# Kernel optimization log

Measured on AMD Instinct MI355X. Metric: run time of the kernel, lower is better.

Reference implementation:

```python
import jax, jax.numpy as jnp
import numpy as np
from jax import lax

DN = ('NCHW', 'OIHW', 'NCHW')

def _conv(x, w, pad):
    return lax.conv_general_dilated(x, w, (1, 1), [(pad, pad), (pad, pad)], dimension_numbers=DN)

def _bn(x, g, b, eps=1e-5):
    # BatchNorm2d in training mode: batch statistics over (N,H,W), biased variance
    m = jnp.mean(x, axis=(0, 2, 3), keepdims=True)
    v = jnp.var(x, axis=(0, 2, 3), keepdims=True)
    return (x - m) * lax.rsqrt(v + eps) * g.reshape(1, -1, 1, 1) + b.reshape(1, -1, 1, 1)

def setup_inputs() -> dict:
    key = jax.random.key(0)
    ks = jax.random.split(key, 24)
    B, H, W = 128, 64, 64
    l_i, lh = 2, (150, 120, 100)
    l_q, cf = 10, H * W
    r = lambda k, s, sc: jax.random.normal(k, s, dtype=jnp.float32) * sc
    return {
        'X': r(ks[0], (B, l_i, H, W), 1.0),
        'obs': r(ks[1], (B, 24), 1.0),
        'h1_w': r(ks[2], (lh[0], l_i, 3, 3), 0.1), 'h1_b': r(ks[3], (lh[0],), 0.05),
        'g1': jnp.ones((lh[0],), jnp.float32), 'b1': jnp.zeros((lh[0],), jnp.float32),
        'h2_w': r(ks[4], (lh[1], lh[0], 3, 3), 0.03), 'h2_b': r(ks[5], (lh[1],), 0.05),
        'g2': jnp.ones((lh[1],), jnp.float32), 'b2': jnp.zeros((lh[1],), jnp.float32),
        'h3_w': r(ks[6], (lh[2], lh[1], 3, 3), 0.03), 'h3_b': r(ks[7], (lh[2],), 0.05),
        'g3': jnp.ones((lh[2],), jnp.float32), 'b3': jnp.zeros((lh[2],), jnp.float32),
        'r_w': r(ks[8], (1, lh[2], 1, 1), 0.1),
        'q_w': r(ks[9], (l_q, 1, 5, 5), 0.1),
        'w': r(ks[10], (l_q, 1, 5, 5), 0.05),  # Parameter (zeros init in torch; randn here for nontrivial math)
        'fc1_w': r(ks[11], (100, 24), 0.1), 'fc1_b': r(ks[12], (100,), 0.05),
        'fc2_w': r(ks[13], (10, 100), 0.1), 'fc2_b': r(ks[14], (10,), 0.05),
        'cv_w': r(ks[15], (1, cf), 0.02), 'cv_b': r(ks[16], (1,), 0.05),
        'K': 36,
    }

def reference(X, obs, h1_w, h1_b, g1, b1, h2_w, h2_b, g2, b2, h3_w, h3_b, g3, b3,
              r_w, q_w, w, fc1_w, fc1_b, fc2_w, fc2_b, cv_w, cv_b, K):
    relu = jax.nn.relu
    h = relu(_bn(_conv(X, h1_w, 1) + h1_b.reshape(1, -1, 1, 1), g1, b1))
    h = relu(_bn(_conv(h, h2_w, 1) + h2_b.reshape(1, -1, 1, 1), g2, b2))
    h = relu(_bn(_conv(h, h3_w, 1) + h3_b.reshape(1, -1, 1, 1), g3, b3))
    r = _conv(h, r_w, 0)                      # [B,1,H,W] reward map
    qr = _conv(r, q_w, 2)                     # conv of r part is constant across VI iterations
    v = jnp.max(qr, axis=1, keepdims=True)    # [B,1,H,W]
    # conv2d(cat([r,v],1), cat([q_w,w],1)) == conv(r,q_w) + conv(v,w)
    def step(v, _):
        q = qr + _conv(v, w, 2)
        return jnp.max(q, axis=1, keepdims=True), None
    # original: K-1 loop iterations + 1 extra conv/max = K total steps after the init
    v, _ = lax.scan(step, v, None, length=K)
    critic = v.reshape(v.shape[0], -1) @ cv_w.T + cv_b
    action_pred = relu(relu(obs @ fc1_w.T + fc1_b) @ fc2_w.T + fc2_b)
    return (critic, action_pred)
```

## Files before the change

### kernel.cpp

```cpp
#include <hip/hip_runtime.h>


#define NHW 524288.0f

typedef __attribute__((ext_vector_type(8))) short v8s;
typedef __attribute__((ext_vector_type(4))) float v4f;

static __device__ __forceinline__ float bf2f(unsigned short u) {
  return __uint_as_float(((unsigned int)u) << 16);
}
static __device__ __forceinline__ unsigned short f2bf(float f) {
  unsigned int x = __float_as_uint(f);
  return (unsigned short)((x + 0x7fffu + ((x >> 16) & 1u)) >> 16);
}
static __device__ __forceinline__ float wave_sum(float s) {
  #pragma unroll
  for (int off = 32; off > 0; off >>= 1) s += __shfl_down(s, off, 64);
  return s;
}

template <int CO, int CI, int CIP>
__global__ __launch_bounds__(256) void repack_w(
    const float* __restrict__ w, unsigned short* __restrict__ Wp)
{
  int i = blockIdx.x * 256 + threadIdx.x;
  const int total = 9 * 128 * CIP;
  if (i >= total) return;
  int pos = i / (128 * CIP);
  int rem = i - pos * (128 * CIP);
  int co  = rem / CIP;
  int ci  = rem - co * CIP;
  float v = (co < CO && ci < CI) ? w[(co * CI + ci) * 9 + pos] : 0.f;
  Wp[i] = f2bf(v);
}

__global__ __launch_bounds__(256) void conv1_stats(
    const float* __restrict__ X, const float* __restrict__ w1,
    const float* __restrict__ b1, float* __restrict__ S, float* __restrict__ Q)
{
  const int tile = blockIdx.x;
  const int b    = tile >> 3;
  const int y0t  = (tile & 7) * 8;
  const int co0  = blockIdx.y * 15;
  const int tid  = threadIdx.x;
  const int x    = tid & 63;
  const int ly0  = (tid >> 6) * 2;

  __shared__ float lin[2][10][66];
  __shared__ float ss[15], qq[15];
  if (tid < 15) { ss[tid] = 0.f; qq[tid] = 0.f; }
  for (int idx = tid; idx < 2 * 10 * 66; idx += 256) {
    int cc = idx / 660, rem = idx - cc * 660;
    int rr = rem / 66,  c   = rem - rr * 66;
    int yy = y0t + rr - 1, xx = c - 1;
    lin[cc][rr][c] = (yy >= 0 && yy < 64 && xx >= 0 && xx < 64)
                         ? X[((size_t)(b * 2 + cc) << 12) + (yy << 6) + xx] : 0.f;
  }
  __syncthreads();

  float iv[2][4][3];
  #pragma unroll
  for (int cc = 0; cc < 2; cc++)
    #pragma unroll
    for (int r = 0; r < 4; r++)
      #pragma unroll
      for (int c = 0; c < 3; c++) iv[cc][r][c] = lin[cc][ly0 + r][x + c];

  #pragma unroll
  for (int co = 0; co < 15; co++) {
    const float* w9 = w1 + (size_t)(co0 + co) * 18;
    float a0 = 0.f, a1 = 0.f;
    #pragma unroll
    for (int cc = 0; cc < 2; cc++)
      #pragma unroll
      for (int ky = 0; ky < 3; ky++)
        #pragma unroll
        for (int kx = 0; kx < 3; kx++) {
          float wv = w9[cc * 9 + ky * 3 + kx];
          a0 = fmaf(iv[cc][ky][kx],     wv, a0);
          a1 = fmaf(iv[cc][ky + 1][kx], wv, a1);
        }
    float bz = b1[co0 + co];
    float t0 = a0 + bz, t1 = a1 + bz;
    float s  = wave_sum(t0 + t1);
    float q  = wave_sum(t0 * t0 + t1 * t1);
    if ((tid & 63) == 0) { atomicAdd(&ss[co], s); atomicAdd(&qq[co], q); }
  }
  __syncthreads();
  if (tid < 15) {
    atomicAdd(&S[co0 + tid], ss[tid]);
    atomicAdd(&Q[co0 + tid], qq[tid]);
  }
}

template <int C>
__global__ void bn_finalize(const float* __restrict__ S, const float* __restrict__ Q,
                            const float* __restrict__ g, const float* __restrict__ be,
                            float* __restrict__ A, float* __restrict__ Bs)
{
  int c = threadIdx.x;
  if (c < C) {
    const float invN = 1.f / NHW;
    float m   = S[c] * invN;
    float var = fmaxf(Q[c] * invN - m * m, 0.f);
    float sc  = g[c] * rsqrtf(var + 1e-5f);
    A[c]  = sc;
    Bs[c] = be[c] - m * sc;
  }
}

__global__ __launch_bounds__(256, 2) void conv2_mfma(
    const float* __restrict__ X,  const float* __restrict__ w1,
    const float* __restrict__ b1f, const float* __restrict__ A1,
    const float* __restrict__ B1, const unsigned short* __restrict__ W2p,
    const float* __restrict__ b2, unsigned short* __restrict__ t2)
{
  const int bx   = blockIdx.x;
  const int b    = bx >> 4;
  const int t16  = bx & 15;
  const int y0   = (t16 >> 2) * 16;
  const int x0   = (t16 & 3) * 16;
  const int cg   = blockIdx.y;
  const int tid  = threadIdx.x;
  const int lane = tid & 63;
  const int wid  = __builtin_amdgcn_readfirstlane(tid >> 6);
  const int ln   = lane & 15;
  const int quad = (lane >> 4) * 8;

  __shared__ __align__(16) float Xs[2][20][20];
  __shared__ float w1s[2700];
  __shared__ float A1s[150], B1s[150], b1s[150], b2s[64];
  __shared__ __align__(16) unsigned short Atile[324 * 34];
  __shared__ __align__(16) unsigned short Btile[9 * 64 * 34];

  for (int i = tid; i < 2700; i += 256) w1s[i] = w1[i];
  for (int i = tid; i < 150; i += 256) { A1s[i] = A1[i]; B1s[i] = B1[i]; b1s[i] = b1f[i]; }
  if (tid < 64) { int co = cg * 64 + tid; b2s[tid] = (co < 120) ? b2[co] : 0.f; }
  for (int i = tid; i < 800; i += 256) {
    int c2 = i / 400, rem = i - c2 * 400;
    int rr = rem / 20, cc = rem - rr * 20;
    int gy = y0 - 2 + rr, gx = x0 - 2 + cc;
    Xs[c2][rr][cc] = (gy >= 0 && gy < 64 && gx >= 0 && gx < 64)
                         ? X[((size_t)(b * 2 + c2) << 12) + (gy << 6) + gx] : 0.f;
  }

  v4f acc[4][4];
  #pragma unroll
  for (int i = 0; i < 4; i++)
    #pragma unroll
    for (int j = 0; j < 4; j++) acc[i][j] = (v4f){0.f, 0.f, 0.f, 0.f};

  for (int chunk = 0; chunk < 5; chunk++) {
    __syncthreads();
    {
      const int ci_loc = tid & 31;
      const int ci = chunk * 32 + ci_loc;
      const bool live = (ci < 150);
      float wv[18], sc = 0.f, sh = 0.f, bz = 0.f;
      if (live) {
        #pragma unroll
        for (int k = 0; k < 18; k++) wv[k] = w1s[ci * 18 + k];
        sc = A1s[ci]; sh = B1s[ci]; bz = b1s[ci];
      }
      for (int pass = 0; pass < 41; pass++) {
        int p = pass * 8 + (tid >> 5);
        if (p < 324) {
          float v = 0.f;
          if (live) {
            int pr = p / 18, pc = p - pr * 18;
            int hy = y0 - 1 + pr, hx = x0 - 1 + pc;
            if (hy >= 0 && hy < 64 && hx >= 0 && hx < 64) {
              float a = bz;
              #pragma unroll
              for (int c2 = 0; c2 < 2; c2++)
                #pragma unroll
                for (int ky = 0; ky < 3; ky++)
                  #pragma unroll
                  for (int kx = 0; kx < 3; kx++)
                    a = fmaf(Xs[c2][pr + ky][pc + kx], wv[c2 * 9 + ky * 3 + kx], a);
              v = fmaxf(fmaf(a, sc, sh), 0.f);
            }
          }
          Atile[p * 34 + ci_loc] = f2bf(v);
        }
      }
    }
    for (int i = tid; i < 2304; i += 256) {
      int pos = i >> 8, rem = i & 255, co = rem >> 2, q = rem & 3;
      uint4 v = *(const uint4*)(W2p + (size_t)(pos * 128 + cg * 64 + co) * 160
                                + chunk * 32 + q * 8);
      *(uint4*)(&Btile[(pos * 64 + co) * 34 + q * 8]) = v;
    }
    __syncthreads();

    v8s afr[6][3];
    #pragma unroll
    for (int t = 0; t < 6; t++)
      #pragma unroll
      for (int kx = 0; kx < 3; kx++)
        afr[t][kx] = *(const v8s*)(&Atile[((wid * 4 + t) * 18 + ln + kx) * 34 + quad]);

    #pragma unroll
    for (int pos = 0; pos < 9; pos++) {
      const int ky = pos / 3, kx = pos - ky * 3;
      v8s bf[4];
      #pragma unroll
      for (int nj = 0; nj < 4; nj++)
        bf[nj] = *(const v8s*)(&Btile[(pos * 64 + nj * 16 + ln) * 34 + quad]);
      #pragma unroll
      for (int mi = 0; mi < 4; mi++) {
        #pragma unroll
        for (int nj = 0; nj < 4; nj++)
          acc[mi][nj] = __builtin_amdgcn_mfma_f32_16x16x32_bf16(
              afr[mi + ky][kx], bf[nj], acc[mi][nj], 0, 0, 0);
      }
    }
  }
  __syncthreads();

  unsigned short* outs = Btile;
  #pragma unroll
  for (int mi = 0; mi < 4; mi++)
    #pragma unroll
    for (int nj = 0; nj < 4; nj++) {
      int n = nj * 16 + ln;
      float bz = b2s[n];
      #pragma unroll
      for (int r2 = 0; r2 < 4; r2++) {
        int m = wid * 64 + mi * 16 + (lane >> 4) * 4 + r2;
        outs[m * 68 + n] = f2bf(acc[mi][nj][r2] + bz);
      }
    }
  __syncthreads();

  const int ng = cg ? 7 : 8;
  for (int i = tid; i < 256 * ng; i += 256) {
    int p = i / ng, g = i - p * ng;
    int gy = y0 + (p >> 4), gx = x0 + (p & 15);
    size_t gpx = ((size_t)b << 12) + (gy << 6) + gx;
    *(uint4*)(t2 + gpx * 120 + cg * 64 + g * 8) = *(const uint4*)(&outs[p * 68 + g * 8]);
  }
}

__global__ __launch_bounds__(256, 2) void conv3_mfma(
    const unsigned short* __restrict__ t2, const float* __restrict__ A2,
    const float* __restrict__ B2, const unsigned short* __restrict__ W3p,
    const float* __restrict__ b3, unsigned short* __restrict__ t3)
{
  const int bx   = blockIdx.x;
  const int b    = bx >> 4;
  const int t16  = bx & 15;
  const int y0   = (t16 >> 2) * 16;
  const int x0   = (t16 & 3) * 16;
  const int cg   = blockIdx.y;
  const int tid  = threadIdx.x;
  const int lane = tid & 63;
  const int wid  = __builtin_amdgcn_readfirstlane(tid >> 6);
  const int ln   = lane & 15;
  const int quad = (lane >> 4) * 8;

  __shared__ float A2s[120], B2s[120], b3s[64];
  __shared__ __align__(16) unsigned short Atile[324 * 34];
  __shared__ __align__(16) unsigned short Btile[9 * 64 * 34];

  for (int i = tid; i < 120; i += 256) { A2s[i] = A2[i]; B2s[i] = B2[i]; }
  if (tid < 64) { int co = cg * 64 + tid; b3s[tid] = (co < 100) ? b3[co] : 0.f; }

  v4f acc[4][4];
  #pragma unroll
  for (int i = 0; i < 4; i++)
    #pragma unroll
    for (int j = 0; j < 4; j++) acc[i][j] = (v4f){0.f, 0.f, 0.f, 0.f};

  for (int chunk = 0; chunk < 4; chunk++) {
    __syncthreads();
    {
      const int ci0 = chunk * 32;
      const int ngr = (chunk == 3) ? 3 : 4;
      for (int i = tid; i < 1296; i += 256) {
        int p = i >> 2, g = i & 3;
        int pr = p / 18, pc = p - pr * 18;
        int hy = y0 - 1 + pr, hx = x0 - 1 + pc;
        union { uint4 v; unsigned short u[8]; } ov;
        ov.v = (uint4){0, 0, 0, 0};
        if (g < ngr && hy >= 0 && hy < 64 && hx >= 0 && hx < 64) {
          size_t gpx = ((size_t)b << 12) + (hy << 6) + hx;
          union { uint4 v; unsigned short u[8]; } in;
          in.v = *(const uint4*)(t2 + gpx * 120 + ci0 + g * 8);
          #pragma unroll
          for (int j = 0; j < 8; j++) {
            int ci = ci0 + g * 8 + j;
            ov.u[j] = f2bf(fmaxf(fmaf(bf2f(in.u[j]), A2s[ci], B2s[ci]), 0.f));
          }
        }
        *(uint4*)(&Atile[p * 34 + g * 8]) = ov.v;
      }
    }
    for (int i = tid; i < 2304; i += 256) {
      int pos = i >> 8, rem = i & 255, co = rem >> 2, q = rem & 3;
      uint4 v = *(const uint4*)(W3p + (size_t)(pos * 128 + cg * 64 + co) * 128
                                + chunk * 32 + q * 8);
      *(uint4*)(&Btile[(pos * 64 + co) * 34 + q * 8]) = v;
    }
    __syncthreads();

    v8s afr[6][3];
    #pragma unroll
    for (int t = 0; t < 6; t++)
      #pragma unroll
      for (int kx = 0; kx < 3; kx++)
        afr[t][kx] = *(const v8s*)(&Atile[((wid * 4 + t) * 18 + ln + kx) * 34 + quad]);

    #pragma unroll
    for (int pos = 0; pos < 9; pos++) {
      const int ky = pos / 3, kx = pos - ky * 3;
      v8s bf[4];
      #pragma unroll
      for (int nj = 0; nj < 4; nj++)
        bf[nj] = *(const v8s*)(&Btile[(pos * 64 + nj * 16 + ln) * 34 + quad]);
      #pragma unroll
      for (int mi = 0; mi < 4; mi++) {
        #pragma unroll
        for (int nj = 0; nj < 4; nj++)
          acc[mi][nj] = __builtin_amdgcn_mfma_f32_16x16x32_bf16(
              afr[mi + ky][kx], bf[nj], acc[mi][nj], 0, 0, 0);
      }
    }
  }
  __syncthreads();

  unsigned short* outs = Btile;
  #pragma unroll
  for (int mi = 0; mi < 4; mi++)
    #pragma unroll
    for (int nj = 0; nj < 4; nj++) {
      int n = nj * 16 + ln;
      float bz = b3s[n];
      #pragma unroll
      for (int r2 = 0; r2 < 4; r2++) {
        int m = wid * 64 + mi * 16 + (lane >> 4) * 4 + r2;
        outs[m * 68 + n] = f2bf(acc[mi][nj][r2] + bz);
      }
    }
  __syncthreads();

  const int ng = cg ? 5 : 8;
  for (int i = tid; i < 256 * ng; i += 256) {
    int p = i / ng, g = i - p * ng;
    int gy = y0 + (p >> 4), gx = x0 + (p & 15);
    size_t gpx = ((size_t)b << 12) + (gy << 6) + gx;
    *(uint4*)(t3 + gpx * 104 + cg * 64 + g * 8) = *(const uint4*)(&outs[p * 68 + g * 8]);
  }
}

template <int ST, int NG, int C>
__global__ __launch_bounds__(256) void nhwc_stats(
    const unsigned short* __restrict__ t, float* __restrict__ S, float* __restrict__ Q)
{
  const int tid = threadIdx.x;
  const int g   = tid & 15;
  const int pl  = tid >> 4;
  const bool valid = (g < NG);
  const int px0 = blockIdx.x * 512;

  __shared__ float ss[128], qq[128];
  for (int i = tid; i < 128; i += 256) { ss[i] = 0.f; qq[i] = 0.f; }
  __syncthreads();

  float s8[8], q8[8];
  #pragma unroll
  for (int j = 0; j < 8; j++) { s8[j] = 0.f; q8[j] = 0.f; }

  if (valid) {
    for (int it = 0; it < 32; it++) {
      size_t px = px0 + it * 16 + pl;
      union { uint4 v; unsigned short u[8]; } in;
      in.v = *(const uint4*)(t + px * ST + g * 8);
      #pragma unroll
      for (int j = 0; j < 8; j++) {
        float v = bf2f(in.u[j]);
        s8[j] += v;
        q8[j] += v * v;
      }
    }
    #pragma unroll
    for (int j = 0; j < 8; j++) {
      atomicAdd(&ss[g * 8 + j], s8[j]);
      atomicAdd(&qq[g * 8 + j], q8[j]);
    }
  }
  __syncthreads();
  if (tid < C) {
    atomicAdd(&S[tid], ss[tid]);
    atomicAdd(&Q[tid], qq[tid]);
  }
}

__global__ __launch_bounds__(256) void bn3_reduce_r(
    const unsigned short* __restrict__ t3, const float* __restrict__ A3,
    const float* __restrict__ B3, const float* __restrict__ rw,
    float* __restrict__ r)
{
  __shared__ float A3s[104], B3s[104], rws[104];
  const int tid = threadIdx.x;
  for (int i = tid; i < 104; i += 256) {
    bool v = (i < 100);
    A3s[i] = v ? A3[i] : 0.f;
    B3s[i] = v ? B3[i] : 0.f;
    rws[i] = v ? rw[i] : 0.f;
  }
  __syncthreads();

  size_t px = (size_t)blockIdx.x * 256 + tid;
  const unsigned short* p = t3 + px * 104;
  float a = 0.f;
  #pragma unroll
  for (int gq = 0; gq < 13; gq++) {
    union { uint4 v; unsigned short u[8]; } in;
    in.v = *(const uint4*)(p + gq * 8);
    #pragma unroll
    for (int j = 0; j < 8; j++) {
      int ci = gq * 8 + j;
      a = fmaf(fmaxf(fmaf(bf2f(in.u[j]), A3s[ci], B3s[ci]), 0.f), rws[ci], a);
    }
  }
  r[px] = a;
}

__global__ __launch_bounds__(256) void qr_init(
    const float* __restrict__ r, const float* __restrict__ qw,
    float* __restrict__ qr, float* __restrict__ v0)
{
  const int tile = blockIdx.x;
  const int b    = tile >> 4;
  const int y0t  = (tile & 15) * 4;
  const int tid  = threadIdx.x;
  const int x    = tid & 63;
  const int ly   = tid >> 6;

  __shared__ float lv[8][68];
  for (int idx = tid; idx < 8 * 68; idx += 256) {
    int rr = idx / 68, c = idx - rr * 68;
    int yy = y0t + rr - 2, xx = c - 2;
    lv[rr][c] = (yy >= 0 && yy < 64 && xx >= 0 && xx < 64)
                    ? r[((size_t)b << 12) + (yy << 6) + xx] : 0.f;
  }
  __syncthreads();

  float iv[5][5];
  #pragma unroll
  for (int ky = 0; ky < 5; ky++)
    #pragma unroll
    for (int kx = 0; kx < 5; kx++) iv[ky][kx] = lv[ly + ky][x + kx];

  const int y = y0t + ly;
  float vmax = -1e30f;
  #pragma unroll
  for (int a = 0; a < 10; a++) {
    float q = 0.f;
    #pragma unroll
    for (int ky = 0; ky < 5; ky++)
      #pragma unroll
      for (int kx = 0; kx < 5; kx++)
        q = fmaf(iv[ky][kx], qw[a * 25 + ky * 5 + kx], q);
    qr[((size_t)(b * 10 + a) << 12) + (y << 6) + x] = q;
    vmax = fmaxf(vmax, q);
  }
  v0[((size_t)b << 12) + (y << 6) + x] = vmax;
}

__global__ __launch_bounds__(256) void vi_step(
    const float* __restrict__ vin, const float* __restrict__ qr,
    const float* __restrict__ ww, float* __restrict__ vout)
{
  const int tile = blockIdx.x;
  const int b    = tile >> 4;
  const int y0t  = (tile & 15) * 4;
  const int tid  = threadIdx.x;
  const int x    = tid & 63;
  const int ly   = tid >> 6;

  __shared__ float lv[8][68];
  for (int idx = tid; idx < 8 * 68; idx += 256) {
    int rr = idx / 68, c = idx - rr * 68;
    int yy = y0t + rr - 2, xx = c - 2;
    lv[rr][c] = (yy >= 0 && yy < 64 && xx >= 0 && xx < 64)
                    ? vin[((size_t)b << 12) + (yy << 6) + xx] : 0.f;
  }
  __syncthreads();

  float iv[5][5];
  #pragma unroll
  for (int ky = 0; ky < 5; ky++)
    #pragma unroll
    for (int kx = 0; kx < 5; kx++) iv[ky][kx] = lv[ly + ky][x + kx];

  const int y = y0t + ly;
  float vmax = -1e30f;
  #pragma unroll
  for (int a = 0; a < 10; a++) {
    float q = qr[((size_t)(b * 10 + a) << 12) + (y << 6) + x];
    #pragma unroll
    for (int ky = 0; ky < 5; ky++)
      #pragma unroll
      for (int kx = 0; kx < 5; kx++)
        q = fmaf(iv[ky][kx], ww[a * 25 + ky * 5 + kx], q);
    vmax = fmaxf(vmax, q);
  }
  vout[((size_t)b << 12) + (y << 6) + x] = vmax;
}

__global__ __launch_bounds__(256) void critic_k(
    const float* __restrict__ v, const float* __restrict__ cvw,
    const float* __restrict__ cvb, float* __restrict__ out)
{
  const int b = blockIdx.x;
  const int tid = threadIdx.x;
  const float4* pv = (const float4*)(v + ((size_t)b << 12));
  const float4* pw = (const float4*)cvw;
  float s = 0.f;
  #pragma unroll
  for (int i = 0; i < 4; i++) {
    float4 a = pv[tid + 256 * i];
    float4 w = pw[tid + 256 * i];
    s += a.x * w.x + a.y * w.y + a.z * w.z + a.w * w.w;
  }
  s = wave_sum(s);
  __shared__ float ls[4];
  const int w = tid >> 6;
  if ((tid & 63) == 0) ls[w] = s;
  __syncthreads();
  if (tid == 0) out[b] = ls[0] + ls[1] + ls[2] + ls[3] + cvb[0];
}

__global__ __launch_bounds__(128) void action_k(
    const float* __restrict__ obs, const float* __restrict__ fc1w,
    const float* __restrict__ fc1b, const float* __restrict__ fc2w,
    const float* __restrict__ fc2b, float* __restrict__ out)
{
  const int b = blockIdx.x;
  const int j = threadIdx.x;
  __shared__ float ob[24];
  __shared__ float h[100];
  if (j < 24) ob[j] = obs[b * 24 + j];
  __syncthreads();
  if (j < 100) {
    float s = fc1b[j];
    #pragma unroll
    for (int k = 0; k < 24; k++) s = fmaf(ob[k], fc1w[j * 24 + k], s);
    h[j] = fmaxf(s, 0.f);
  }
  __syncthreads();
  if (j < 10) {
    float s = fc2b[j];
    for (int k = 0; k < 100; k++) s = fmaf(h[k], fc2w[j * 100 + k], s);
    out[128 + b * 10 + j] = fmaxf(s, 0.f);
  }
}

extern "C" void kernel_launch(void* const* d_in, const int* in_sizes, int n_in,
                              void* d_out, int out_size, void* d_ws,
                              size_t ws_size, hipStream_t stream)
{
  const float* X     = (const float*)d_in[0];
  const float* obs   = (const float*)d_in[1];
  const float* h1_w  = (const float*)d_in[2];
  const float* h1_b  = (const float*)d_in[3];
  const float* g1    = (const float*)d_in[4];
  const float* b1    = (const float*)d_in[5];
  const float* h2_w  = (const float*)d_in[6];
  const float* h2_b  = (const float*)d_in[7];
  const float* g2    = (const float*)d_in[8];
  const float* b2    = (const float*)d_in[9];
  const float* h3_w  = (const float*)d_in[10];
  const float* h3_b  = (const float*)d_in[11];
  const float* g3    = (const float*)d_in[12];
  const float* b3    = (const float*)d_in[13];
  const float* r_w   = (const float*)d_in[14];
  const float* q_w   = (const float*)d_in[15];
  const float* w_vi  = (const float*)d_in[16];
  const float* fc1_w = (const float*)d_in[17];
  const float* fc1_b = (const float*)d_in[18];
  const float* fc2_w = (const float*)d_in[19];
  const float* fc2_b = (const float*)d_in[20];
  const float* cv_w  = (const float*)d_in[21];
  const float* cv_b  = (const float*)d_in[22];

  char* ws = (char*)d_ws;
  unsigned short* t2  = (unsigned short*)ws;
  unsigned short* t3  = (unsigned short*)(ws + 125829120ull);
  unsigned short* W2p = (unsigned short*)(ws + 234881024ull);
  unsigned short* W3p = (unsigned short*)(ws + 235249664ull);
  float*          ST  = (float*)         (ws + 235544576ull);
  float* S1 = ST +    0; float* Q1 = ST +  150; float* A1 = ST +  300; float* B1 = ST +  450;
  float* S2 = ST +  600; float* Q2 = ST +  720; float* A2 = ST +  840; float* B2 = ST +  960;
  float* S3 = ST + 1080; float* Q3 = ST + 1180; float* A3 = ST + 1280; float* B3 = ST + 1380;
  float* r  = (float*)ws;
  float* qr = r + 524288;
  float* vA = qr + 5242880;
  float* vB = vA + 524288;

  hipMemsetAsync(ST, 0, 1480 * sizeof(float), stream);

  repack_w<120, 150, 160><<<720, 256, 0, stream>>>(h2_w, W2p);
  repack_w<100, 120, 128><<<576, 256, 0, stream>>>(h3_w, W3p);

  conv1_stats<<<dim3(1024, 10), 256, 0, stream>>>(X, h1_w, h1_b, S1, Q1);
  bn_finalize<150><<<1, 256, 0, stream>>>(S1, Q1, g1, b1, A1, B1);

  conv2_mfma<<<dim3(2048, 2), 256, 0, stream>>>(X, h1_w, h1_b, A1, B1, W2p, h2_b, t2);
  nhwc_stats<120, 15, 120><<<1024, 256, 0, stream>>>(t2, S2, Q2);
  bn_finalize<120><<<1, 256, 0, stream>>>(S2, Q2, g2, b2, A2, B2);

  conv3_mfma<<<dim3(2048, 2), 256, 0, stream>>>(t2, A2, B2, W3p, h3_b, t3);
  nhwc_stats<104, 13, 100><<<1024, 256, 0, stream>>>(t3, S3, Q3);
  bn_finalize<100><<<1, 256, 0, stream>>>(S3, Q3, g3, b3, A3, B3);

  bn3_reduce_r<<<2048, 256, 0, stream>>>(t3, A3, B3, r_w, r);

  qr_init<<<2048, 256, 0, stream>>>(r, q_w, qr, vA);
  for (int i = 0; i < 36; i++) {
    const float* vin = (i & 1) ? vB : vA;
    float* vout      = (i & 1) ? vA : vB;
    vi_step<<<2048, 256, 0, stream>>>(vin, qr, w_vi, vout);
  }

  float* out = (float*)d_out;
  critic_k<<<128, 256, 0, stream>>>(vA, cv_w, cv_b, out);
  action_k<<<128, 128, 0, stream>>>(obs, fc1_w, fc1_b, fc2_w, fc2_b, out);
}
```

Before: 1.547 ms.

## Compute all output channels per block in conv2/conv3, read weights directly from global

```diff
diff --git a/kernel.cpp b/kernel.cpp
--- a/kernel.cpp
+++ b/kernel.cpp
@@ -120,7 +120,6 @@
   const int t16  = bx & 15;
   const int y0   = (t16 >> 2) * 16;
   const int x0   = (t16 & 3) * 16;
-  const int cg   = blockIdx.y;
   const int tid  = threadIdx.x;
   const int lane = tid & 63;
   const int wid  = __builtin_amdgcn_readfirstlane(tid >> 6);
@@ -129,13 +128,13 @@
 
   __shared__ __align__(16) float Xs[2][20][20];
   __shared__ float w1s[2700];
-  __shared__ float A1s[150], B1s[150], b1s[150], b2s[64];
+  __shared__ float A1s[150], B1s[150], b1s[150], b2s[128];
   __shared__ __align__(16) unsigned short Atile[324 * 34];
-  __shared__ __align__(16) unsigned short Btile[9 * 64 * 34];
+  __shared__ __align__(16) unsigned short outs[256 * 68];
 
   for (int i = tid; i < 2700; i += 256) w1s[i] = w1[i];
   for (int i = tid; i < 150; i += 256) { A1s[i] = A1[i]; B1s[i] = B1[i]; b1s[i] = b1f[i]; }
-  if (tid < 64) { int co = cg * 64 + tid; b2s[tid] = (co < 120) ? b2[co] : 0.f; }
+  if (tid < 128) b2s[tid] = (tid < 120) ? b2[tid] : 0.f;
   for (int i = tid; i < 800; i += 256) {
     int c2 = i / 400, rem = i - c2 * 400;
     int rr = rem / 20, cc = rem - rr * 20;
@@ -144,11 +143,11 @@
                          ? X[((size_t)(b * 2 + c2) << 12) + (gy << 6) + gx] : 0.f;
   }
 
-  v4f acc[4][4];
+  v4f acc[4][8];
   #pragma unroll
   for (int i = 0; i < 4; i++)
     #pragma unroll
-    for (int j = 0; j < 4; j++) acc[i][j] = (v4f){0.f, 0.f, 0.f, 0.f};
+    for (int j = 0; j < 8; j++) acc[i][j] = (v4f){0.f, 0.f, 0.f, 0.f};
 
   for (int chunk = 0; chunk < 5; chunk++) {
     __syncthreads();
@@ -185,12 +184,6 @@
         }
       }
     }
-    for (int i = tid; i < 2304; i += 256) {
-      int pos = i >> 8, rem = i & 255, co = rem >> 2, q = rem & 3;
-      uint4 v = *(const uint4*)(W2p + (size_t)(pos * 128 + cg * 64 + co) * 160
-                                + chunk * 32 + q * 8);
-      *(uint4*)(&Btile[(pos * 64 + co) * 34 + q * 8]) = v;
-    }
     __syncthreads();
 
     v8s afr[6][3];
@@ -203,42 +196,46 @@
     #pragma unroll
     for (int pos = 0; pos < 9; pos++) {
       const int ky = pos / 3, kx = pos - ky * 3;
-      v8s bf[4];
-      #pragma unroll
-      for (int nj = 0; nj < 4; nj++)
-        bf[nj] = *(const v8s*)(&Btile[(pos * 64 + nj * 16 + ln) * 34 + quad]);
+      const unsigned short* bw =
+          W2p + (size_t)(pos * 128 + ln) * 160 + chunk * 32 + quad;
+      v8s bf[8];
+      #pragma unroll
+      for (int nj = 0; nj < 8; nj++)
+        bf[nj] = *(const v8s*)(bw + (size_t)nj * 16 * 160);
       #pragma unroll
       for (int mi = 0; mi < 4; mi++) {
         #pragma unroll
-        for (int nj = 0; nj < 4; nj++)
+        for (int nj = 0; nj < 8; nj++)
           acc[mi][nj] = __builtin_amdgcn_mfma_f32_16x16x32_bf16(
               afr[mi + ky][kx], bf[nj], acc[mi][nj], 0, 0, 0);
       }
     }
   }
-  __syncthreads();
-
-  unsigned short* outs = Btile;
-  #pragma unroll
-  for (int mi = 0; mi < 4; mi++)
-    #pragma unroll
-    for (int nj = 0; nj < 4; nj++) {
-      int n = nj * 16 + ln;
-      float bz = b2s[n];
-      #pragma unroll
-      for (int r2 = 0; r2 < 4; r2++) {
-        int m = wid * 64 + mi * 16 + (lane >> 4) * 4 + r2;
-        outs[m * 68 + n] = f2bf(acc[mi][nj][r2] + bz);
-      }
-    }
-  __syncthreads();
-
-  const int ng = cg ? 7 : 8;
-  for (int i = tid; i < 256 * ng; i += 256) {
-    int p = i / ng, g = i - p * ng;
-    int gy = y0 + (p >> 4), gx = x0 + (p & 15);
-    size_t gpx = ((size_t)b << 12) + (gy << 6) + gx;
-    *(uint4*)(t2 + gpx * 120 + cg * 64 + g * 8) = *(const uint4*)(&outs[p * 68 + g * 8]);
+
+  #pragma unroll
+  for (int half = 0; half < 2; half++) {
+    __syncthreads();
+    #pragma unroll
+    for (int mi = 0; mi < 4; mi++)
+      #pragma unroll
+      for (int njl = 0; njl < 4; njl++) {
+        int n = njl * 16 + ln;
+        float bz = b2s[half * 64 + n];
+        #pragma unroll
+        for (int r2 = 0; r2 < 4; r2++) {
+          int m = wid * 64 + mi * 16 + (lane >> 4) * 4 + r2;
+          outs[m * 68 + n] = f2bf(acc[mi][half * 4 + njl][r2] + bz);
+        }
+      }
+    __syncthreads();
+    const int ng = half ? 7 : 8;
+    for (int i = tid; i < 256 * ng; i += 256) {
+      int p = i / ng, g = i - p * ng;
+      int gy = y0 + (p >> 4), gx = x0 + (p & 15);
+      size_t gpx = ((size_t)b << 12) + (gy << 6) + gx;
+      *(uint4*)(t2 + gpx * 120 + half * 64 + g * 8) =
+          *(const uint4*)(&outs[p * 68 + g * 8]);
+    }
   }
 }
 
@@ -252,25 +249,24 @@
   const int t16  = bx & 15;
   const int y0   = (t16 >> 2) * 16;
   const int x0   = (t16 & 3) * 16;
-  const int cg   = blockIdx.y;
   const int tid  = threadIdx.x;
   const int lane = tid & 63;
   const int wid  = __builtin_amdgcn_readfirstlane(tid >> 6);
   const int ln   = lane & 15;
   const int quad = (lane >> 4) * 8;
 
-  __shared__ float A2s[120], B2s[120], b3s[64];
+  __shared__ float A2s[120], B2s[120], b3s[128];
   __shared__ __align__(16) unsigned short Atile[324 * 34];
-  __shared__ __align__(16) unsigned short Btile[9 * 64 * 34];
+  __shared__ __align__(16) unsigned short outs[256 * 68];
 
   for (int i = tid; i < 120; i += 256) { A2s[i] = A2[i]; B2s[i] = B2[i]; }
-  if (tid < 64) { int co = cg * 64 + tid; b3s[tid] = (co < 100) ? b3[co] : 0.f; }
-
-  v4f acc[4][4];
+  if (tid < 128) b3s[tid] = (tid < 100) ? b3[tid] : 0.f;
+
+  v4f acc[4][8];
   #pragma unroll
   for (int i = 0; i < 4; i++)
     #pragma unroll
-    for (int j = 0; j < 4; j++) acc[i][j] = (v4f){0.f, 0.f, 0.f, 0.f};
+    for (int j = 0; j < 8; j++) acc[i][j] = (v4f){0.f, 0.f, 0.f, 0.f};
 
   for (int chunk = 0; chunk < 4; chunk++) {
     __syncthreads();
@@ -296,12 +292,6 @@
         *(uint4*)(&Atile[p * 34 + g * 8]) = ov.v;
       }
     }
-    for (int i = tid; i < 2304; i += 256) {
-      int pos = i >> 8, rem = i & 255, co = rem >> 2, q = rem & 3;
-      uint4 v = *(const uint4*)(W3p + (size_t)(pos * 128 + cg * 64 + co) * 128
-                                + chunk * 32 + q * 8);
-      *(uint4*)(&Btile[(pos * 64 + co) * 34 + q * 8]) = v;
-    }
     __syncthreads();
 
     v8s afr[6][3];
@@ -314,42 +304,46 @@
     #pragma unroll
     for (int pos = 0; pos < 9; pos++) {
       const int ky = pos / 3, kx = pos - ky * 3;
-      v8s bf[4];
-      #pragma unroll
-      for (int nj = 0; nj < 4; nj++)
-        bf[nj] = *(const v8s*)(&Btile[(pos * 64 + nj * 16 + ln) * 34 + quad]);
+      const unsigned short* bw =
+          W3p + (size_t)(pos * 128 + ln) * 128 + chunk * 32 + quad;
+      v8s bf[8];
+      #pragma unroll
+      for (int nj = 0; nj < 8; nj++)
+        bf[nj] = *(const v8s*)(bw + (size_t)nj * 16 * 128);
       #pragma unroll
       for (int mi = 0; mi < 4; mi++) {
         #pragma unroll
-        for (int nj = 0; nj < 4; nj++)
+        for (int nj = 0; nj < 8; nj++)
           acc[mi][nj] = __builtin_amdgcn_mfma_f32_16x16x32_bf16(
               afr[mi + ky][kx], bf[nj], acc[mi][nj], 0, 0, 0);
       }
     }
   }
-  __syncthreads();
-
-  unsigned short* outs = Btile;
-  #pragma unroll
-  for (int mi = 0; mi < 4; mi++)
-    #pragma unroll
-    for (int nj = 0; nj < 4; nj++) {
-      int n = nj * 16 + ln;
-      float bz = b3s[n];
-      #pragma unroll
-      for (int r2 = 0; r2 < 4; r2++) {
-        int m = wid * 64 + mi * 16 + (lane >> 4) * 4 + r2;
-        outs[m * 68 + n] = f2bf(acc[mi][nj][r2] + bz);
-      }
-    }
-  __syncthreads();
-
-  const int ng = cg ? 5 : 8;
-  for (int i = tid; i < 256 * ng; i += 256) {
-    int p = i / ng, g = i - p * ng;
-    int gy = y0 + (p >> 4), gx = x0 + (p & 15);
-    size_t gpx = ((size_t)b << 12) + (gy << 6) + gx;
-    *(uint4*)(t3 + gpx * 104 + cg * 64 + g * 8) = *(const uint4*)(&outs[p * 68 + g * 8]);
+
+  #pragma unroll
+  for (int half = 0; half < 2; half++) {
+    __syncthreads();
+    #pragma unroll
+    for (int mi = 0; mi < 4; mi++)
+      #pragma unroll
+      for (int njl = 0; njl < 4; njl++) {
+        int n = njl * 16 + ln;
+        float bz = b3s[half * 64 + n];
+        #pragma unroll
+        for (int r2 = 0; r2 < 4; r2++) {
+          int m = wid * 64 + mi * 16 + (lane >> 4) * 4 + r2;
+          outs[m * 68 + n] = f2bf(acc[mi][half * 4 + njl][r2] + bz);
+        }
+      }
+    __syncthreads();
+    const int ng = half ? 5 : 8;
+    for (int i = tid; i < 256 * ng; i += 256) {
+      int p = i / ng, g = i - p * ng;
+      int gy = y0 + (p >> 4), gx = x0 + (p & 15);
+      size_t gpx = ((size_t)b << 12) + (gy << 6) + gx;
+      *(uint4*)(t3 + gpx * 104 + half * 64 + g * 8) =
+          *(const uint4*)(&outs[p * 68 + g * 8]);
+    }
   }
 }
 
@@ -608,11 +602,11 @@
   conv1_stats<<<dim3(1024, 10), 256, 0, stream>>>(X, h1_w, h1_b, S1, Q1);
   bn_finalize<150><<<1, 256, 0, stream>>>(S1, Q1, g1, b1, A1, B1);
 
-  conv2_mfma<<<dim3(2048, 2), 256, 0, stream>>>(X, h1_w, h1_b, A1, B1, W2p, h2_b, t2);
+  conv2_mfma<<<2048, 256, 0, stream>>>(X, h1_w, h1_b, A1, B1, W2p, h2_b, t2);
   nhwc_stats<120, 15, 120><<<1024, 256, 0, stream>>>(t2, S2, Q2);
   bn_finalize<120><<<1, 256, 0, stream>>>(S2, Q2, g2, b2, A2, B2);
 
-  conv3_mfma<<<dim3(2048, 2), 256, 0, stream>>>(t2, A2, B2, W3p, h3_b, t3);
+  conv3_mfma<<<2048, 256, 0, stream>>>(t2, A2, B2, W3p, h3_b, t3);
   nhwc_stats<104, 13, 100><<<1024, 256, 0, stream>>>(t3, S3, Q3);
   bn_finalize<100><<<1, 256, 0, stream>>>(S3, Q3, g3, b3, A3, B3);
 
```

Result: faster. 1.319 ms (-14.8%).
